# Optimization experiments

Hardware: AMD Instinct MI355X
Metric: run time of the kernel (lower is better)

The kernel has to match this reference:

```python
import jax, jax.numpy as jnp
import numpy as np

B, S, DIM = 2, 2048, 4096
HQ, HKV, HD = 32, 8, 128
N_REP = HQ // HKV
MAX_S = 2048
ROPE_BASE = 10000.0


def rotate_half(x):
    half = x.shape[-1] // 2
    return jnp.concatenate([-x[..., half:], x[..., :half]], axis=-1)


def setup_inputs() -> dict:
    key = jax.random.key(0)
    ks = jax.random.split(key, 8)
    x = jax.random.normal(ks[0], (B, S, DIM), dtype=jnp.float32)
    Wq = jax.random.normal(ks[1], (HQ * HD, DIM), dtype=jnp.float32) * 0.02
    bq = jax.random.normal(ks[2], (HQ * HD,), dtype=jnp.float32) * 0.02
    Wk = jax.random.normal(ks[3], (HKV * HD, DIM), dtype=jnp.float32) * 0.02
    bk = jax.random.normal(ks[4], (HKV * HD,), dtype=jnp.float32) * 0.02
    Wv = jax.random.normal(ks[5], (HKV * HD, DIM), dtype=jnp.float32) * 0.02
    bv = jax.random.normal(ks[6], (HKV * HD,), dtype=jnp.float32) * 0.02
    Wo = jax.random.normal(ks[7], (DIM, HQ * HD), dtype=jnp.float32) * 0.02
    # RoPE tables (HF convention: angles duplicated across both halves)
    inv_freq = 1.0 / (ROPE_BASE ** (jnp.arange(0, HD, 2, dtype=jnp.float32) / HD))
    pos = jnp.arange(S, dtype=jnp.float32)
    ang = pos[:, None] * inv_freq[None, :]              # [S, HD/2]
    emb = jnp.concatenate([ang, ang], axis=-1)          # [S, HD]
    cos, sin = jnp.cos(emb), jnp.sin(emb)
    # static KV cache, zero-initialized as in the module
    cache_k = jnp.zeros((B, HKV, MAX_S, HD), dtype=jnp.float32)
    cache_v = jnp.zeros((B, HKV, MAX_S, HD), dtype=jnp.float32)
    # causal additive mask
    causal = jnp.tril(jnp.ones((S, S), dtype=bool))
    mask = jnp.where(causal, 0.0, -1e9).astype(jnp.float32)[None, None]  # [1,1,S,S]
    return {"x": x, "cos": cos, "sin": sin, "Wq": Wq, "bq": bq, "Wk": Wk,
            "bk": bk, "Wv": Wv, "bv": bv, "Wo": Wo, "cache_k": cache_k,
            "cache_v": cache_v, "mask": mask, "start_pos": 0}


def reference(x, cos, sin, Wq, bq, Wk, bk, Wv, bv, Wo, cache_k, cache_v, mask, start_pos):
    bsz, seqlen, _ = x.shape
    scaling = 1.0 / jnp.sqrt(jnp.float32(HD))
    # QKV projections
    xq = (jnp.einsum('bsd,ed->bse', x, Wq) + bq).reshape(bsz, seqlen, HQ, HD).transpose(0, 2, 1, 3)
    xk = (jnp.einsum('bsd,ed->bse', x, Wk) + bk).reshape(bsz, seqlen, HKV, HD).transpose(0, 2, 1, 3)
    xv = (jnp.einsum('bsd,ed->bse', x, Wv) + bv).reshape(bsz, seqlen, HKV, HD).transpose(0, 2, 1, 3)
    # RoPE
    c = cos[None, None]  # [1,1,S,HD]
    s = sin[None, None]
    xq = xq * c + rotate_half(xq) * s
    xk = xk * c + rotate_half(xk) * s
    # static KV-cache append + slice (start_pos is a Python int)
    cache_k = jax.lax.dynamic_update_slice(cache_k, xk, (0, 0, start_pos, 0))
    cache_v = jax.lax.dynamic_update_slice(cache_v, xv, (0, 0, start_pos, 0))
    keys = cache_k[:, :, :start_pos + seqlen]     # [B,HKV,K,HD]
    values = cache_v[:, :, :start_pos + seqlen]
    # GQA: repeat kv heads (repeat_interleave over head dim)
    keys = jnp.repeat(keys, N_REP, axis=1)        # [B,HQ,K,HD]
    values = jnp.repeat(values, N_REP, axis=1)
    # SDPA with additive mask
    scores = jnp.einsum('bhqd,bhkd->bhqk', xq, keys) * scaling + mask
    attn = jax.nn.softmax(scores, axis=-1)
    out = jnp.einsum('bhqk,bhkd->bhqd', attn, values)
    out = out.transpose(0, 2, 1, 3).reshape(bsz, seqlen, HQ * HD)
    return jnp.einsum('bse,de->bsd', out, Wo)
```

## Files before the change

### kernel.cpp

```cpp
#include <hip/hip_runtime.h>

typedef _Float16 half8 __attribute__((ext_vector_type(8)));
typedef _Float16 half4 __attribute__((ext_vector_type(4)));
typedef float floatx4 __attribute__((ext_vector_type(4)));
typedef float floatx16 __attribute__((ext_vector_type(16)));

#define SWZ(r) ((((r) & 7) << 1) | (((r) >> 3) & 1))

__device__ __forceinline__ void gld16(const void* g, void* l) {
  __builtin_amdgcn_global_load_lds(
      (const __attribute__((address_space(1))) unsigned int*)g,
      (__attribute__((address_space(3))) unsigned int*)l, 16, 0, 0);
}

__global__ void convert_all(const float* __restrict__ x, const float* __restrict__ Wq,
                            const float* __restrict__ Wk, const float* __restrict__ Wv,
                            const float* __restrict__ Wo, const float* __restrict__ bq,
                            const float* __restrict__ bk, const float* __restrict__ bv,
                            _Float16* __restrict__ xb, _Float16* __restrict__ wqkv,
                            _Float16* __restrict__ wo_b, float* __restrict__ biasc) {
  long i = (long)blockIdx.x * 256 + threadIdx.x;
  const long N0 = 2097152, N1 = N0 + 2097152, N2 = N1 + 524288, N3 = N2 + 524288,
             N4 = N3 + 2097152;
  const float* s;
  _Float16* d;
  long j;
  if (i < N0) { s = x; d = xb; j = i; }
  else if (i < N1) { s = Wq; d = wqkv; j = i - N0; }
  else if (i < N2) { s = Wk; d = wqkv + (size_t)4096 * 4096; j = i - N1; }
  else if (i < N3) { s = Wv; d = wqkv + (size_t)5120 * 4096; j = i - N2; }
  else if (i < N4) { s = Wo; d = wo_b; j = i - N3; }
  else {
    long k = i - N4;
    if (k < 4096) biasc[k] = bq[k];
    else if (k < 5120) biasc[k] = bk[k - 4096];
    else if (k < 6144) biasc[k] = bv[k - 5120];
    return;
  }
  float4 a = ((const float4*)s)[2 * j];
  float4 b2 = ((const float4*)s)[2 * j + 1];
  half8 h;
  h[0] = (_Float16)a.x; h[1] = (_Float16)a.y; h[2] = (_Float16)a.z; h[3] = (_Float16)a.w;
  h[4] = (_Float16)b2.x; h[5] = (_Float16)b2.y; h[6] = (_Float16)b2.z; h[7] = (_Float16)b2.w;
  ((half8*)d)[j] = h;
}

template <typename OutT, bool HasBias>
__global__ __launch_bounds__(256) void gemm_bt(const _Float16* __restrict__ A,
                                               const _Float16* __restrict__ B,
                                               const float* __restrict__ bias,
                                               OutT* __restrict__ C, int M, int N, int K) {
  __shared__ _Float16 as[128 * 64];
  __shared__ _Float16 bs[128 * 64];
  const int tid = threadIdx.x;
  const int w = tid >> 6, lane = tid & 63;
  const int quad = lane >> 4, l16 = lane & 15;
  const int M0 = blockIdx.y * 128, N0 = blockIdx.x * 128;
  const int wm = (w >> 1) * 64, wn = (w & 1) * 64;

  floatx4 acc[4][4];
#pragma unroll
  for (int i = 0; i < 4; ++i)
#pragma unroll
    for (int j = 0; j < 4; ++j) acc[i][j] = (floatx4){0.f, 0.f, 0.f, 0.f};

  const int sr = tid >> 3, g0 = tid & 7;
  const int csw = (g0 ^ (sr & 7)) * 8;
  const _Float16* Ag[4];
  const _Float16* Bg[4];
  _Float16* asd[4];
  _Float16* bsd[4];
#pragma unroll
  for (int c = 0; c < 4; ++c) {
    Ag[c] = A + (size_t)(M0 + c * 32 + sr) * K + csw;
    Bg[c] = B + (size_t)(N0 + c * 32 + sr) * K + csw;
    asd[c] = &as[(c * 32 + w * 8) * 64];
    bsd[c] = &bs[(c * 32 + w * 8) * 64];
  }

  int aoff[4][2], boff[4][2];
#pragma unroll
  for (int mi = 0; mi < 4; ++mi)
#pragma unroll
    for (int kd = 0; kd < 2; ++kd) {
      int ra = wm + mi * 16 + l16;
      aoff[mi][kd] = ra * 64 + (((kd * 4 + quad) ^ (ra & 7)) * 8);
      int rb = wn + mi * 16 + l16;
      boff[mi][kd] = rb * 64 + (((kd * 4 + quad) ^ (rb & 7)) * 8);
    }

  for (int kk = 0; kk < K; kk += 64) {
    __syncthreads();
#pragma unroll
    for (int c = 0; c < 4; ++c) gld16(Ag[c] + kk, asd[c]);
#pragma unroll
    for (int c = 0; c < 4; ++c) gld16(Bg[c] + kk, bsd[c]);
    __syncthreads();
#pragma unroll
    for (int kd = 0; kd < 2; ++kd) {
      half8 af[4], bf[4];
#pragma unroll
      for (int i = 0; i < 4; ++i) af[i] = *(const half8*)&as[aoff[i][kd]];
#pragma unroll
      for (int i = 0; i < 4; ++i) bf[i] = *(const half8*)&bs[boff[i][kd]];
#pragma unroll
      for (int mi = 0; mi < 4; ++mi)
#pragma unroll
        for (int ni = 0; ni < 4; ++ni)
          acc[mi][ni] = __builtin_amdgcn_mfma_f32_16x16x32_f16(af[mi], bf[ni], acc[mi][ni], 0, 0, 0);
    }
  }

#pragma unroll
  for (int mi = 0; mi < 4; ++mi)
#pragma unroll
    for (int ni = 0; ni < 4; ++ni) {
      int row = M0 + wm + mi * 16 + quad * 4;
      int col = N0 + wn + ni * 16 + l16;
      float bvv = HasBias ? bias[col] : 0.f;
#pragma unroll
      for (int r = 0; r < 4; ++r) {
        float v = acc[mi][ni][r] + bvv;
        C[(size_t)(row + r) * N + col] = (OutT)v;
      }
    }
}

__global__ void rope_qk(const _Float16* __restrict__ qkv, const float* __restrict__ cosb,
                        const float* __restrict__ sinb, _Float16* __restrict__ q_r,
                        _Float16* __restrict__ k_r) {
  int t = blockIdx.x * 256 + threadIdx.x;
  int d = t & 63;
  int r = t >> 6;
  int hh = r % 40;
  int r2 = r / 40;
  int s = r2 & 2047;
  int b = r2 >> 11;
  size_t mrow = (size_t)(b * 2048 + s) * 6144;
  float c = cosb[s * 128 + d], sn = sinb[s * 128 + d];
  if (hh < 32) {
    size_t base = mrow + hh * 128 + d;
    float x1 = (float)qkv[base], x2 = (float)qkv[base + 64];
    const float sc = 0.12751744737079736f;
    float o1 = (x1 * c - x2 * sn) * sc;
    float o2 = (x2 * c + x1 * sn) * sc;
    size_t ob = ((size_t)((b * 32 + hh) * 2048 + s)) * 128 + d;
    q_r[ob] = (_Float16)o1;
    q_r[ob + 64] = (_Float16)o2;
  } else {
    int hk = hh - 32;
    size_t base = mrow + 4096 + hk * 128 + d;
    float x1 = (float)qkv[base], x2 = (float)qkv[base + 64];
    float o1 = x1 * c - x2 * sn;
    float o2 = x2 * c + x1 * sn;
    size_t ob = ((size_t)((b * 8 + hk) * 2048 + s)) * 128 + d;
    k_r[ob] = (_Float16)o1;
    k_r[ob + 64] = (_Float16)o2;
  }
}

__global__ void v_transpose(const _Float16* __restrict__ qkv, _Float16* __restrict__ v_t) {
  __shared__ _Float16 tile[32][33];
  int st = blockIdx.x * 32, dt = blockIdx.y * 32, bh = blockIdx.z;
  int tx = threadIdx.x & 31, ty = threadIdx.x >> 5;
  int b = bh >> 3, hv = bh & 7;
#pragma unroll
  for (int j = 0; j < 4; ++j) {
    int s = st + ty + j * 8;
    tile[ty + j * 8][tx] = qkv[(size_t)(b * 2048 + s) * 6144 + 5120 + hv * 128 + dt + tx];
  }
  __syncthreads();
#pragma unroll
  for (int j = 0; j < 4; ++j)
    v_t[((size_t)bh * 128 + dt + ty + j * 8) * 2048 + st + tx] = tile[tx][ty + j * 8];
}

__global__ __launch_bounds__(256, 2) void attn_kernel(const _Float16* __restrict__ q_r,
                                                      const _Float16* __restrict__ k_r,
                                                      const _Float16* __restrict__ v_t,
                                                      _Float16* __restrict__ att) {
  __shared__ __align__(16) _Float16 kt[128 * 128];
  __shared__ __align__(16) _Float16 vt[128 * 128];
  const int tid = threadIdx.x;
  const int w = tid >> 6, lane = tid & 63;
  const int l32 = lane & 31, hi = lane >> 5;
  const int qb = 15 - blockIdx.x;
  const int h = blockIdx.y, b = blockIdx.z;
  const int q0 = qb * 128;
  const _Float16* qh = q_r + ((size_t)(b * 32 + h) * 2048) * 128;
  const _Float16* kh = k_r + ((size_t)(b * 8 + (h >> 2)) * 2048) * 128;
  const _Float16* vh = v_t + ((size_t)(b * 8 + (h >> 2)) * 128) * 2048;

  const int ql = w * 32 + l32;
  const int myq = q0 + ql;
  const int swq = SWZ(ql);
  const int swl = SWZ(l32);

  half8 bq[8];
#pragma unroll
  for (int kd = 0; kd < 8; ++kd)
    bq[kd] = *(const half8*)&qh[(size_t)myq * 128 + kd * 16 + hi * 8];

  floatx16 oacc[4];
#pragma unroll
  for (int di = 0; di < 4; ++di)
#pragma unroll
    for (int j = 0; j < 16; ++j) oacc[di][j] = 0.f;
  float mrun = -1e30f, lrun = 0.f;

  const int srow0 = tid >> 4, sgrp = tid & 15;

  for (int kti = 0; kti <= qb; ++kti) {
    __syncthreads();
    const _Float16* kg = kh + (size_t)kti * 128 * 128;
#pragma unroll
    for (int c = 0; c < 8; ++c) {
      int row = srow0 + c * 16;
      int gc = (sgrp ^ SWZ(row)) * 8;
      gld16(kg + row * 128 + gc, &kt[w * 512 + c * 2048]);
    }
#pragma unroll
    for (int c = 0; c < 8; ++c) {
      int row = srow0 + c * 16;
      int gc = (sgrp ^ SWZ(row)) * 8;
      gld16(vh + (size_t)row * 2048 + kti * 128 + gc, &vt[w * 512 + c * 2048]);
    }
    __syncthreads();

    floatx16 sacc[4];
#pragma unroll
    for (int ni = 0; ni < 4; ++ni)
#pragma unroll
      for (int j = 0; j < 16; ++j) sacc[ni][j] = 0.f;
#pragma unroll
    for (int ni = 0; ni < 4; ++ni) {
      int rb = (ni * 32 + l32) * 128;
#pragma unroll
      for (int kd = 0; kd < 8; ++kd) {
        half8 ka = *(const half8*)&kt[rb + (((kd * 2 + hi) ^ swl) * 8)];
        sacc[ni] = __builtin_amdgcn_mfma_f32_32x32x16_f16(ka, bq[kd], sacc[ni], 0, 0, 0);
      }
    }

    if (kti == qb) {
#pragma unroll
      for (int ni = 0; ni < 4; ++ni)
#pragma unroll
        for (int g = 0; g < 4; ++g) {
          int kvb = kti * 128 + ni * 32 + g * 8 + hi * 4;
#pragma unroll
          for (int t = 0; t < 4; ++t)
            if (kvb + t > myq) sacc[ni][g * 4 + t] = -1e30f;
        }
    }

    float tm = -1e30f;
#pragma unroll
    for (int ni = 0; ni < 4; ++ni)
#pragma unroll
      for (int j = 0; j < 16; ++j) tm = fmaxf(tm, sacc[ni][j]);
    tm = fmaxf(tm, __shfl_xor(tm, 32));
    float nm = fmaxf(mrun, tm);
    float al = exp2f(mrun - nm);
    mrun = nm;
    float ts = 0.f;
#pragma unroll
    for (int ni = 0; ni < 4; ++ni)
#pragma unroll
      for (int j = 0; j < 16; ++j) {
        float p = exp2f(sacc[ni][j] - nm);
        sacc[ni][j] = p;
        ts += p;
      }
    ts += __shfl_xor(ts, 32);
    lrun = lrun * al + ts;
#pragma unroll
    for (int di = 0; di < 4; ++di)
#pragma unroll
      for (int j = 0; j < 16; ++j) oacc[di][j] *= al;

    __syncthreads();

#pragma unroll
    for (int ni = 0; ni < 4; ++ni)
#pragma unroll
      for (int g = 0; g < 4; ++g) {
        half4 p4;
#pragma unroll
        for (int t = 0; t < 4; ++t) p4[t] = (_Float16)sacc[ni][g * 4 + t];
        *(half4*)&kt[ql * 128 + (((ni * 4 + g) ^ swq) * 8) + hi * 4] = p4;
      }

#pragma unroll
    for (int ks = 0; ks < 8; ++ks) {
      half8 pb = *(const half8*)&kt[ql * 128 + (((ks * 2 + hi) ^ swq) * 8)];
#pragma unroll
      for (int di = 0; di < 4; ++di) {
        int rv = (di * 32 + l32) * 128;
        half8 va = *(const half8*)&vt[rv + (((ks * 2 + hi) ^ swl) * 8)];
        oacc[di] = __builtin_amdgcn_mfma_f32_32x32x16_f16(va, pb, oacc[di], 0, 0, 0);
      }
    }
  }

  float inv = 1.f / lrun;
  _Float16* ob = att + ((size_t)b * 2048 + myq) * 4096 + h * 128;
#pragma unroll
  for (int di = 0; di < 4; ++di)
#pragma unroll
    for (int g = 0; g < 4; ++g) {
      half4 o4;
#pragma unroll
      for (int t = 0; t < 4; ++t) o4[t] = (_Float16)(oacc[di][g * 4 + t] * inv);
      *(half4*)&ob[di * 32 + g * 8 + hi * 4] = o4;
    }
}

extern "C" void kernel_launch(void* const* d_in, const int* in_sizes, int n_in, void* d_out,
                              int out_size, void* d_ws, size_t ws_size, hipStream_t stream) {
  const float* x = (const float*)d_in[0];
  const float* cosb = (const float*)d_in[1];
  const float* sinb = (const float*)d_in[2];
  const float* Wq = (const float*)d_in[3];
  const float* bq = (const float*)d_in[4];
  const float* Wk = (const float*)d_in[5];
  const float* bk = (const float*)d_in[6];
  const float* Wv = (const float*)d_in[7];
  const float* bv = (const float*)d_in[8];
  const float* Wo = (const float*)d_in[9];
  float* out = (float*)d_out;

  char* p = (char*)d_ws;
  _Float16* xb = (_Float16*)p;   p += (size_t)4096 * 4096 * 2;
  _Float16* wqkv = (_Float16*)p; p += (size_t)6144 * 4096 * 2;
  _Float16* wo_b = (_Float16*)p; p += (size_t)4096 * 4096 * 2;
  _Float16* qkv = (_Float16*)p;  p += (size_t)4096 * 6144 * 2;
  _Float16* q_r = (_Float16*)p;  p += (size_t)2 * 32 * 2048 * 128 * 2;
  _Float16* k_r = (_Float16*)p;  p += (size_t)2 * 8 * 2048 * 128 * 2;
  _Float16* v_t = (_Float16*)p;  p += (size_t)2 * 8 * 128 * 2048 * 2;
  _Float16* att = (_Float16*)p;  p += (size_t)4096 * 4096 * 2;
  float* biasc = (float*)p;      p += 6144 * 4;

  convert_all<<<28696, 256, 0, stream>>>(x, Wq, Wk, Wv, Wo, bq, bk, bv, xb, wqkv, wo_b, biasc);

  gemm_bt<_Float16, true><<<dim3(48, 32), 256, 0, stream>>>(xb, wqkv, biasc, qkv, 4096, 6144, 4096);
  rope_qk<<<40960, 256, 0, stream>>>(qkv, cosb, sinb, q_r, k_r);
  v_transpose<<<dim3(64, 4, 16), 256, 0, stream>>>(qkv, v_t);
  attn_kernel<<<dim3(16, 32, 2), 256, 0, stream>>>(q_r, k_r, v_t, att);
  gemm_bt<float, false><<<dim3(32, 32), 256, 0, stream>>>(att, wo_b, nullptr, out, 4096, 4096, 4096);
}
```

Measured before the change: 937.7 us.

## Replace GEMM with 256x256 double-buffered 8-wave pipelined kernel

Replaces the 128x128 single-buffered GEMM with a 256x256-tile, 512-thread kernel that double-buffers A and B in LDS. Global-to-LDS loads for the next k-tile are interleaved with MFMA phases, using explicit waitcnt, barriers and setprio. The aim is to hide memory latency and raise per-block data reuse for both the QKV and output projections. In exchange it uses 128KB of LDS per block and far fewer blocks (384 and 256), which may underfill 256 CUs and leave a tail wave.

```diff
diff --git a/kernel.cpp b/kernel.cpp
--- a/kernel.cpp
+++ b/kernel.cpp
@@ -46,84 +46,139 @@
 }
 
 template <typename OutT, bool HasBias>
-__global__ __launch_bounds__(256) void gemm_bt(const _Float16* __restrict__ A,
-                                               const _Float16* __restrict__ B,
-                                               const float* __restrict__ bias,
-                                               OutT* __restrict__ C, int M, int N, int K) {
-  __shared__ _Float16 as[128 * 64];
-  __shared__ _Float16 bs[128 * 64];
+__global__ __launch_bounds__(512, 2) void gemm256(const _Float16* __restrict__ A,
+                                                  const _Float16* __restrict__ B,
+                                                  const float* __restrict__ bias,
+                                                  OutT* __restrict__ C, int M, int N, int K) {
+  __shared__ _Float16 as[2][256 * 64];
+  __shared__ _Float16 bs[2][256 * 64];
   const int tid = threadIdx.x;
   const int w = tid >> 6, lane = tid & 63;
   const int quad = lane >> 4, l16 = lane & 15;
-  const int M0 = blockIdx.y * 128, N0 = blockIdx.x * 128;
-  const int wm = (w >> 1) * 64, wn = (w & 1) * 64;
-
-  floatx4 acc[4][4];
-#pragma unroll
-  for (int i = 0; i < 4; ++i)
+  const int sw7 = l16 & 7;
+  const int M0 = blockIdx.y * 256, N0 = blockIdx.x * 256;
+  const int wm = (w >> 2) * 128, wn = (w & 3) * 64;
+  const int NT = K >> 6;
+
+  floatx4 acc[8][4];
+#pragma unroll
+  for (int i = 0; i < 8; ++i)
 #pragma unroll
     for (int j = 0; j < 4; ++j) acc[i][j] = (floatx4){0.f, 0.f, 0.f, 0.f};
 
-  const int sr = tid >> 3, g0 = tid & 7;
-  const int csw = (g0 ^ (sr & 7)) * 8;
+  const int sr = tid >> 3;
+  const int csw = ((tid & 7) ^ (sr & 7)) * 8;
   const _Float16* Ag[4];
   const _Float16* Bg[4];
-  _Float16* asd[4];
-  _Float16* bsd[4];
-#pragma unroll
-  for (int c = 0; c < 4; ++c) {
-    Ag[c] = A + (size_t)(M0 + c * 32 + sr) * K + csw;
-    Bg[c] = B + (size_t)(N0 + c * 32 + sr) * K + csw;
-    asd[c] = &as[(c * 32 + w * 8) * 64];
-    bsd[c] = &bs[(c * 32 + w * 8) * 64];
-  }
-
-  int aoff[4][2], boff[4][2];
-#pragma unroll
-  for (int mi = 0; mi < 4; ++mi)
-#pragma unroll
-    for (int kd = 0; kd < 2; ++kd) {
-      int ra = wm + mi * 16 + l16;
-      aoff[mi][kd] = ra * 64 + (((kd * 4 + quad) ^ (ra & 7)) * 8);
-      int rb = wn + mi * 16 + l16;
-      boff[mi][kd] = rb * 64 + (((kd * 4 + quad) ^ (rb & 7)) * 8);
-    }
-
-  for (int kk = 0; kk < K; kk += 64) {
-    __syncthreads();
-#pragma unroll
-    for (int c = 0; c < 4; ++c) gld16(Ag[c] + kk, asd[c]);
-#pragma unroll
-    for (int c = 0; c < 4; ++c) gld16(Bg[c] + kk, bsd[c]);
-    __syncthreads();
-#pragma unroll
-    for (int kd = 0; kd < 2; ++kd) {
-      half8 af[4], bf[4];
-#pragma unroll
-      for (int i = 0; i < 4; ++i) af[i] = *(const half8*)&as[aoff[i][kd]];
-#pragma unroll
-      for (int i = 0; i < 4; ++i) bf[i] = *(const half8*)&bs[boff[i][kd]];
-#pragma unroll
-      for (int mi = 0; mi < 4; ++mi)
-#pragma unroll
-        for (int ni = 0; ni < 4; ++ni)
-          acc[mi][ni] = __builtin_amdgcn_mfma_f32_16x16x32_f16(af[mi], bf[ni], acc[mi][ni], 0, 0, 0);
-    }
-  }
-
-#pragma unroll
-  for (int mi = 0; mi < 4; ++mi)
+#pragma unroll
+  for (int j = 0; j < 4; ++j) {
+    Ag[j] = A + (size_t)(M0 + j * 64 + sr) * K + csw;
+    Bg[j] = B + (size_t)(N0 + j * 64 + sr) * K + csw;
+  }
+
+#define STA(p, t, j) gld16(Ag[j] + (size_t)(t) * 64, &as[p][(j) * 4096 + w * 512])
+#define STB(p, t, j) gld16(Bg[j] + (size_t)(t) * 64, &bs[p][(j) * 4096 + w * 512])
+
+#define FRA(p, q, mi, kd) \
+  (*(const half8*)&as[p][(wm + (q) * 32 + (mi) * 16 + l16) * 64 + ((((kd) * 4 + quad) ^ sw7) * 8)])
+#define FRB(p, ni, kd) \
+  (*(const half8*)&bs[p][(wn + (ni) * 16 + l16) * 64 + ((((kd) * 4 + quad) ^ sw7) * 8)])
+
+#define LD_A(p, q)                                   \
+  _Pragma("unroll") for (int kd = 0; kd < 2; ++kd)   \
+  _Pragma("unroll") for (int mi = 0; mi < 2; ++mi)   \
+      af[mi][kd] = FRA(p, q, mi, kd);
+
+#define LD_B(p)                                      \
+  _Pragma("unroll") for (int kd = 0; kd < 2; ++kd)   \
+  _Pragma("unroll") for (int ni = 0; ni < 4; ++ni)   \
+      bf[ni][kd] = FRB(p, ni, kd);
+
+#define PH_COMPUTE(q)                                                                  \
+  __builtin_amdgcn_s_barrier();                                                        \
+  asm volatile("s_waitcnt lgkmcnt(0)" ::: "memory");                                   \
+  __builtin_amdgcn_sched_barrier(0);                                                   \
+  __builtin_amdgcn_s_setprio(1);                                                       \
+  _Pragma("unroll") for (int kd = 0; kd < 2; ++kd)                                     \
+  _Pragma("unroll") for (int mi = 0; mi < 2; ++mi)                                     \
+  _Pragma("unroll") for (int ni = 0; ni < 4; ++ni)                                     \
+      acc[(q) * 2 + mi][ni] = __builtin_amdgcn_mfma_f32_16x16x32_f16(                  \
+          af[mi][kd], bf[ni][kd], acc[(q) * 2 + mi][ni], 0, 0, 0);                     \
+  __builtin_amdgcn_s_setprio(0);
+
+  half8 bf[4][2], af[2][2];
+
+  STA(0, 0, 0); STA(0, 0, 1); STA(0, 0, 2); STA(0, 0, 3);
+  STB(0, 0, 0); STB(0, 0, 1); STB(0, 0, 2); STB(0, 0, 3);
+  STB(1, 1, 0); STB(1, 1, 1); STB(1, 1, 2); STB(1, 1, 3);
+  asm volatile("s_waitcnt vmcnt(4)" ::: "memory");
+  __builtin_amdgcn_s_barrier();
+
+  for (int t = 0; t < NT; t += 2) {
+    const int t2 = (t + 2 < NT) ? t + 2 : t;
+    const int t3 = (t + 3 < NT) ? t + 3 : t + 1;
+
+    LD_B(0); LD_A(0, 0);
+    STA(1, t + 1, 0); STA(1, t + 1, 1); STA(1, t + 1, 2); STA(1, t + 1, 3);
+    PH_COMPUTE(0);
+    __builtin_amdgcn_s_barrier();
+
+    LD_A(0, 1);
+    STB(0, t2, 0); STB(0, t2, 1);
+    PH_COMPUTE(1);
+    __builtin_amdgcn_s_barrier();
+
+    LD_A(0, 2);
+    STB(0, t2, 2); STB(0, t2, 3);
+    PH_COMPUTE(2);
+    __builtin_amdgcn_s_barrier();
+
+    LD_A(0, 3);
+    PH_COMPUTE(3);
+    asm volatile("s_waitcnt vmcnt(4)" ::: "memory");
+    __builtin_amdgcn_sched_barrier(0);
+    __builtin_amdgcn_s_barrier();
+
+    LD_B(1); LD_A(1, 0);
+    STA(0, t2, 0); STA(0, t2, 1);
+    PH_COMPUTE(0);
+    __builtin_amdgcn_s_barrier();
+
+    LD_A(1, 1);
+    STA(0, t2, 2); STA(0, t2, 3);
+    PH_COMPUTE(1);
+    __builtin_amdgcn_s_barrier();
+
+    LD_A(1, 2);
+    STB(1, t3, 0); STB(1, t3, 1);
+    PH_COMPUTE(2);
+    __builtin_amdgcn_s_barrier();
+
+    LD_A(1, 3);
+    STB(1, t3, 2); STB(1, t3, 3);
+    PH_COMPUTE(3);
+    asm volatile("s_waitcnt vmcnt(4)" ::: "memory");
+    __builtin_amdgcn_sched_barrier(0);
+    __builtin_amdgcn_s_barrier();
+  }
+
+#pragma unroll
+  for (int mf = 0; mf < 8; ++mf)
 #pragma unroll
     for (int ni = 0; ni < 4; ++ni) {
-      int row = M0 + wm + mi * 16 + quad * 4;
+      int row = M0 + wm + mf * 16 + quad * 4;
       int col = N0 + wn + ni * 16 + l16;
       float bvv = HasBias ? bias[col] : 0.f;
 #pragma unroll
-      for (int r = 0; r < 4; ++r) {
-        float v = acc[mi][ni][r] + bvv;
-        C[(size_t)(row + r) * N + col] = (OutT)v;
-      }
-    }
+      for (int r = 0; r < 4; ++r) C[(size_t)(row + r) * N + col] = (OutT)(acc[mf][ni][r] + bvv);
+    }
+#undef STA
+#undef STB
+#undef FRA
+#undef FRB
+#undef LD_A
+#undef LD_B
+#undef PH_COMPUTE
 }
 
 __global__ void rope_qk(const _Float16* __restrict__ qkv, const float* __restrict__ cosb,
@@ -343,9 +398,9 @@
 
   convert_all<<<28696, 256, 0, stream>>>(x, Wq, Wk, Wv, Wo, bq, bk, bv, xb, wqkv, wo_b, biasc);
 
-  gemm_bt<_Float16, true><<<dim3(48, 32), 256, 0, stream>>>(xb, wqkv, biasc, qkv, 4096, 6144, 4096);
+  gemm256<_Float16, true><<<dim3(24, 16), 512, 0, stream>>>(xb, wqkv, biasc, qkv, 4096, 6144, 4096);
   rope_qk<<<40960, 256, 0, stream>>>(qkv, cosb, sinb, q_r, k_r);
   v_transpose<<<dim3(64, 4, 16), 256, 0, stream>>>(qkv, v_t);
   attn_kernel<<<dim3(16, 32, 2), 256, 0, stream>>>(q_r, k_r, v_t, att);
-  gemm_bt<float, false><<<dim3(32, 32), 256, 0, stream>>>(att, wo_b, nullptr, out, 4096, 4096, 4096);
-}
+  gemm256<float, false><<<dim3(16, 16), 512, 0, stream>>>(att, wo_b, nullptr, out, 4096, 4096, 4096);
+}
```

New measurement: 928.4 us. Within noise of the previous version (-1.0%).
